# Kernel optimization log

Hardware: AMD Instinct MI355X
Metric: run time of the kernel (lower is better)

Reference implementation:

```python
import jax, jax.numpy as jnp
import numpy as np

B, T, M, P = 64, 2048, 512, 512


def setup_inputs() -> dict:
    key = jax.random.key(0)
    ks = jax.random.split(key, 9)
    s = 0.02
    return {
        "hidden_state": jax.random.normal(ks[0], (B, P), jnp.float32),
        "cell_state": jax.random.normal(ks[1], (B, P), jnp.float32),
        "encoder_h": jax.random.normal(ks[2], (B, T, M), jnp.float32),
        # Dense W_d: (2p -> m)
        "W_d": jax.random.normal(ks[3], (2 * P, M), jnp.float32) * s,
        "b_wd": jnp.zeros((M,), jnp.float32),
        # Dense U_d: (m -> m)
        "U_d": jax.random.normal(ks[4], (M, M), jnp.float32) * s,
        "b_ud": jnp.zeros((M,), jnp.float32),
        # Dense v_d: (m -> 1)
        "v_d": jax.random.normal(ks[5], (M, 1), jnp.float32) * s,
        "b_vd": jnp.zeros((1,), jnp.float32),
    }


def reference(hidden_state, cell_state, encoder_h, W_d, b_wd, U_d, b_ud, v_d, b_vd):
    # W_d(RepeatVector(T)(concat([d, s]))): the Dense is applied to the same
    # (B, 2p) vector at every time step, so compute it once and broadcast.
    ds = jnp.concatenate([hidden_state, cell_state], axis=-1)          # (B, 2p)
    ds_proj = ds @ W_d + b_wd                                          # (B, m)
    enc_proj = jnp.einsum('btm,mn->btn', encoder_h, U_d) + b_ud        # (B, T, m)
    e = jnp.tanh(ds_proj[:, None, :] + enc_proj)                       # (B, T, m)
    l = e @ v_d + b_vd                                                 # (B, T, 1)
    return jax.nn.softmax(l, axis=1)                                   # softmax over T
```

## Files before the change

### kernel.cpp

```cpp
#include <hip/hip_runtime.h>
#include <cstdint>
#include <cstddef>


typedef float  floatx4 __attribute__((ext_vector_type(4)));
typedef short  shortx8 __attribute__((ext_vector_type(8)));
typedef unsigned int uintx4 __attribute__((ext_vector_type(4)));

__device__ __forceinline__ short f2bf_rne(float f) {
  unsigned u = __float_as_uint(f);
  unsigned r = u + 0x7FFFu + ((u >> 16) & 1u);
  return (short)(r >> 16);
}

__device__ __forceinline__ unsigned pack_bf_trunc(float lo, float hi) {
  return __builtin_amdgcn_perm(__float_as_uint(hi), __float_as_uint(lo), 0x07060302u);
}

#define SB() __builtin_amdgcn_sched_barrier(0)
#define WAIT_VM0() asm volatile("s_waitcnt vmcnt(0)" ::: "memory")
#define WAIT_VM4() asm volatile("s_waitcnt vmcnt(4)" ::: "memory")
#define WAIT_VM8() asm volatile("s_waitcnt vmcnt(8)" ::: "memory")
#define WAIT_LGKM0() asm volatile("s_waitcnt lgkmcnt(0)" ::: "memory")
#define BAR() __builtin_amdgcn_s_barrier()

extern "C" __global__ __launch_bounds__(256) void prep_kernel(
    const float* __restrict__ hidden, const float* __restrict__ cell,
    const float* __restrict__ W_d, const float* __restrict__ b_wd,
    const float* __restrict__ U_d, const float* __restrict__ b_ud,
    float* __restrict__ S, short* __restrict__ UT, float* __restrict__ lzero)
{
  int bx = blockIdx.x, tid = threadIdx.x;
  if (bx < 128) {
    int idx = bx * 256 + tid;
    int b = idx >> 9, n = idx & 511;
    const float* h = hidden + b * 512;
    const float* c = cell   + b * 512;
    float a0 = b_wd[n] + b_ud[n], a1 = 0.f, a2 = 0.f, a3 = 0.f;
    for (int k = 0; k < 512; k += 4) {
      a0 = fmaf(h[k + 0], W_d[(k + 0) * 512 + n], a0);
      a1 = fmaf(h[k + 1], W_d[(k + 1) * 512 + n], a1);
      a2 = fmaf(h[k + 2], W_d[(k + 2) * 512 + n], a2);
      a3 = fmaf(h[k + 3], W_d[(k + 3) * 512 + n], a3);
    }
    for (int k = 0; k < 512; k += 4) {
      a0 = fmaf(c[k + 0], W_d[(k + 512) * 512 + n], a0);
      a1 = fmaf(c[k + 1], W_d[(k + 513) * 512 + n], a1);
      a2 = fmaf(c[k + 2], W_d[(k + 514) * 512 + n], a2);
      a3 = fmaf(c[k + 3], W_d[(k + 515) * 512 + n], a3);
    }
    S[idx] = (a0 + a1) + (a2 + a3);
  } else if (bx < 384) {
    int idx = (bx - 128) * 1024 + tid * 4;
    int n = idx >> 9, k0 = idx & 511;
    unsigned lo = (unsigned short)f2bf_rne(U_d[(size_t)(k0 + 0) * 512 + n]) |
                  ((unsigned)(unsigned short)f2bf_rne(U_d[(size_t)(k0 + 1) * 512 + n]) << 16);
    unsigned hi = (unsigned short)f2bf_rne(U_d[(size_t)(k0 + 2) * 512 + n]) |
                  ((unsigned)(unsigned short)f2bf_rne(U_d[(size_t)(k0 + 3) * 512 + n]) << 16);
    uint2 w; w.x = lo; w.y = hi;
    *(uint2*)(UT + idx) = w;
  } else {
    int idx = ((bx - 384) * 256 + tid) * 4;
    floatx4 z = {0.f, 0.f, 0.f, 0.f};
    *(floatx4*)(lzero + idx) = z;
  }
}

struct GemmState {
  short (*As)[4096];
  const float* aptr;
  const short* bfp[4];
  int afrag0, awbase;
};

template <int T>
__device__ __forceinline__ void kiter(
    GemmState& st, shortx8 (&bfr)[2][4][2], floatx4 (&areg)[4],
    floatx4 (&acc)[4][4])
{
  constexpr int CUR = T & 1;
  constexpr int NXT = CUR ^ 1;
  const short* Ab = &st.As[CUR][0];
  shortx8 af[4][2];

#pragma unroll
  for (int tr = 0; tr < 4; ++tr)
#pragma unroll
    for (int s = 0; s < 2; ++s)
      af[tr][s] = *(const shortx8*)(Ab + ((st.afrag0 + tr * 1024) ^ (s * 32)));
  SB();
  if constexpr (T < 7) {
#pragma unroll
    for (int tc = 0; tc < 4; ++tc)
#pragma unroll
      for (int s = 0; s < 2; ++s)
        bfr[NXT][tc][s] = *(const shortx8*)(st.bfp[tc] + (T + 1) * 64 + s * 32);
  }
  SB();
  WAIT_LGKM0(); SB();
  __builtin_amdgcn_s_setprio(1);
#pragma unroll
  for (int tr = 0; tr < 2; ++tr)
#pragma unroll
    for (int tc = 0; tc < 4; ++tc)
#pragma unroll
      for (int s = 0; s < 2; ++s)
        acc[tr][tc] = __builtin_amdgcn_mfma_f32_16x16x32_bf16(
            af[tr][s], bfr[CUR][tc][s], acc[tr][tc], 0, 0, 0);
  __builtin_amdgcn_s_setprio(0);
  SB();
  if constexpr (T < 7) {
    WAIT_VM8(); SB();
    short* An = &st.As[NXT][0];
    uintx4 w0, w1;
    w0.x = pack_bf_trunc(areg[0].x, areg[0].y);
    w0.y = pack_bf_trunc(areg[0].z, areg[0].w);
    w0.z = pack_bf_trunc(areg[1].x, areg[1].y);
    w0.w = pack_bf_trunc(areg[1].z, areg[1].w);
    w1.x = pack_bf_trunc(areg[2].x, areg[2].y);
    w1.y = pack_bf_trunc(areg[2].z, areg[2].w);
    w1.z = pack_bf_trunc(areg[3].x, areg[3].y);
    w1.w = pack_bf_trunc(areg[3].z, areg[3].w);
    *(uintx4*)(An + st.awbase)       = w0;
    *(uintx4*)(An + (st.awbase ^ 8)) = w1;
    SB();
  }
  if constexpr (T < 6) {
#pragma unroll
    for (int i = 0; i < 4; ++i)
      areg[i] = *(const floatx4*)(st.aptr + (T + 2) * 64 + i * 4);
  }
  SB();
  __builtin_amdgcn_s_setprio(1);
#pragma unroll
  for (int tr = 2; tr < 4; ++tr)
#pragma unroll
    for (int tc = 0; tc < 4; ++tc)
#pragma unroll
      for (int s = 0; s < 2; ++s)
        acc[tr][tc] = __builtin_amdgcn_mfma_f32_16x16x32_bf16(
            af[tr][s], bfr[CUR][tc][s], acc[tr][tc], 0, 0, 0);
  __builtin_amdgcn_s_setprio(0);
  SB();
  if constexpr (T < 7) {
    if constexpr (T < 6) { WAIT_VM4(); }
    else                 { WAIT_VM0(); }
    SB();
    WAIT_LGKM0(); SB();
    BAR(); SB();
  }
}

extern "C" __global__ __launch_bounds__(256, 2) void attn_gemm(
    const float* __restrict__ A, const short* __restrict__ UT,
    const float* __restrict__ S, const float* __restrict__ vd,
    float* __restrict__ lout)
{
  __shared__ short As[2][4096];

  const int tid = threadIdx.x;
  const int bx  = blockIdx.x;
  const int xcd = bx & 7;
  const int wg  = xcd * 512 + (bx >> 3);
  const int cb  = wg & 1;
  const int rb  = wg >> 1;
  const int row0 = rb << 6;
  const int col0 = cb << 8;
  const int lane = tid & 63;
  const int wc = tid >> 6;
  const int q = lane >> 4, l15 = lane & 15;

  GemmState st;
  st.As = As;

  const int arow = tid >> 2;
  const int akq  = tid & 3;
  st.aptr   = A + (size_t)(row0 + arow) * 512 + akq * 16;
  st.awbase = arow * 64 + (((2 * akq) ^ (arow & 7)) << 3);

#pragma unroll
  for (int tc = 0; tc < 4; ++tc)
    st.bfp[tc] = UT + (size_t)(col0 + wc * 64 + tc * 16 + l15) * 512 + q * 8;

  st.afrag0 = l15 * 64 + ((q ^ (l15 & 7)) << 3);

  floatx4 acc[4][4];
#pragma unroll
  for (int i = 0; i < 4; ++i)
#pragma unroll
    for (int j = 0; j < 4; ++j)
      acc[i][j] = (floatx4){0.f, 0.f, 0.f, 0.f};

  floatx4 areg[4];
  shortx8 bfr[2][4][2];

  SB();
#pragma unroll
  for (int i = 0; i < 4; ++i) areg[i] = *(const floatx4*)(st.aptr + i * 4);
  SB();
#pragma unroll
  for (int tc = 0; tc < 4; ++tc)
#pragma unroll
    for (int s = 0; s < 2; ++s)
      bfr[0][tc][s] = *(const shortx8*)(st.bfp[tc] + s * 32);
  SB();
  WAIT_VM8(); SB();
  {
    uintx4 w0, w1;
    w0.x = pack_bf_trunc(areg[0].x, areg[0].y);
    w0.y = pack_bf_trunc(areg[0].z, areg[0].w);
    w0.z = pack_bf_trunc(areg[1].x, areg[1].y);
    w0.w = pack_bf_trunc(areg[1].z, areg[1].w);
    w1.x = pack_bf_trunc(areg[2].x, areg[2].y);
    w1.y = pack_bf_trunc(areg[2].z, areg[2].w);
    w1.z = pack_bf_trunc(areg[3].x, areg[3].y);
    w1.w = pack_bf_trunc(areg[3].z, areg[3].w);
    *(uintx4*)(&As[0][st.awbase])       = w0;
    *(uintx4*)(&As[0][st.awbase ^ 8])   = w1;
  }
  SB();
#pragma unroll
  for (int i = 0; i < 4; ++i) areg[i] = *(const floatx4*)(st.aptr + 64 + i * 4);
  SB();
  WAIT_VM4(); SB();
  WAIT_LGKM0(); SB();
  BAR(); SB();

  kiter<0>(st, bfr, areg, acc);
  kiter<1>(st, bfr, areg, acc);
  kiter<2>(st, bfr, areg, acc);
  kiter<3>(st, bfr, areg, acc);
  kiter<4>(st, bfr, areg, acc);
  kiter<5>(st, bfr, areg, acc);
  kiter<6>(st, bfr, areg, acc);
  kiter<7>(st, bfr, areg, acc);

  const int bb = rb >> 5;
  const float* Srow = S + bb * 512;
  float sv[4], vv[4];
#pragma unroll
  for (int tc = 0; tc < 4; ++tc) {
    int n = col0 + wc * 64 + tc * 16 + l15;
    sv[tc] = Srow[n];
    vv[tc] = vd[n];
  }
#pragma unroll
  for (int tr = 0; tr < 4; ++tr) {
#pragma unroll
    for (int r = 0; r < 4; ++r) {
      float ssum = 0.f;
#pragma unroll
      for (int tc = 0; tc < 4; ++tc) {
        float x = acc[tr][tc][r] + sv[tc];
        x = fminf(15.f, fmaxf(-15.f, x));
        float e2 = __expf(2.f * x);
        float e = (e2 - 1.f) / (e2 + 1.f);
        ssum += e * vv[tc];
      }
      ssum += __shfl_xor(ssum, 1);
      ssum += __shfl_xor(ssum, 2);
      ssum += __shfl_xor(ssum, 4);
      ssum += __shfl_xor(ssum, 8);
      if (l15 == 0) {
        int row = row0 + tr * 16 + q * 4 + r;
        atomicAdd(lout + row, ssum);
      }
    }
  }
}

extern "C" __global__ __launch_bounds__(256) void softmax_t(float* __restrict__ l)
{
  int b = blockIdx.x, tid = threadIdx.x;
  int wave = tid >> 6, lane = tid & 63;
  float* row = l + (size_t)b * 2048;
  float v[8];
  float mx = -3.4e38f;
#pragma unroll
  for (int i = 0; i < 8; ++i) { v[i] = row[tid + i * 256]; mx = fmaxf(mx, v[i]); }
#pragma unroll
  for (int m = 1; m < 64; m <<= 1) mx = fmaxf(mx, __shfl_xor(mx, m));
  __shared__ float red[8];
  if (lane == 0) red[wave] = mx;
  __syncthreads();
  mx = fmaxf(fmaxf(red[0], red[1]), fmaxf(red[2], red[3]));
  float s = 0.f;
#pragma unroll
  for (int i = 0; i < 8; ++i) { v[i] = __expf(v[i] - mx); s += v[i]; }
#pragma unroll
  for (int m = 1; m < 64; m <<= 1) s += __shfl_xor(s, m);
  if (lane == 0) red[4 + wave] = s;
  __syncthreads();
  s = red[4] + red[5] + red[6] + red[7];
  float inv = 1.f / s;
#pragma unroll
  for (int i = 0; i < 8; ++i) row[tid + i * 256] = v[i] * inv;
}

extern "C" void kernel_launch(void* const* d_in, const int* in_sizes, int n_in,
                              void* d_out, int out_size, void* d_ws, size_t ws_size,
                              hipStream_t stream) {
  const float* hidden = (const float*)d_in[0];
  const float* cell   = (const float*)d_in[1];
  const float* enc    = (const float*)d_in[2];
  const float* W_d    = (const float*)d_in[3];
  const float* b_wd   = (const float*)d_in[4];
  const float* U_d    = (const float*)d_in[5];
  const float* b_ud   = (const float*)d_in[6];
  const float* v_d    = (const float*)d_in[7];
  float* out = (float*)d_out;
  float* S   = (float*)d_ws;
  short* UT  = (short*)((char*)d_ws + 32768 * sizeof(float));

  hipLaunchKernelGGL(prep_kernel, dim3(512), dim3(256), 0, stream,
                     hidden, cell, W_d, b_wd, U_d, b_ud, S, UT, out);
  hipLaunchKernelGGL(attn_gemm, dim3(4096), dim3(256), 0, stream,
                     enc, UT, S, v_d, out);
  hipLaunchKernelGGL(softmax_t, dim3(64), dim3(256), 0, stream, out);
}
```

Baseline: 502.4 us.

## Enlarge GEMM tile to 128x256 with LDS-staged B via global_load_lds

The attention GEMM block grows from 256 to 512 threads and now covers 128 rows instead of 64, so each B (U_d bf16) tile is reused across two wave-rows. B is staged through LDS with direct global-to-LDS loads, replacing the per-wave register prefetch from global memory. The prep kernel writes U_d pre-tiled and pre-swizzled so the LDS copy needs no reshuffling. A fp32 registers are now double-buffered. The goal is to cut redundant global/L2 traffic for B. The cost is 96KB of LDS per block, which likely limits occupancy, plus more complex wait-count sequencing.

Measured after the change: 528.0 us. +5.1%, slower.

```diff
diff --git a/kernel.cpp b/kernel.cpp
--- a/kernel.cpp
+++ b/kernel.cpp
@@ -16,6 +16,11 @@
 __device__ __forceinline__ unsigned pack_bf_trunc(float lo, float hi) {
   return __builtin_amdgcn_perm(__float_as_uint(hi), __float_as_uint(lo), 0x07060302u);
 }
+
+#define GLOAD_LDS16(gptr, lptr)                                                 \
+  __builtin_amdgcn_global_load_lds(                                             \
+      (const __attribute__((address_space(1))) void*)(gptr),                    \
+      (__attribute__((address_space(3))) void*)(lptr), 16, 0, 0)
 
 #define SB() __builtin_amdgcn_sched_barrier(0)
 #define WAIT_VM0() asm volatile("s_waitcnt vmcnt(0)" ::: "memory")
@@ -51,12 +56,20 @@
     }
     S[idx] = (a0 + a1) + (a2 + a3);
   } else if (bx < 384) {
-    int idx = (bx - 128) * 1024 + tid * 4;
-    int n = idx >> 9, k0 = idx & 511;
-    unsigned lo = (unsigned short)f2bf_rne(U_d[(size_t)(k0 + 0) * 512 + n]) |
-                  ((unsigned)(unsigned short)f2bf_rne(U_d[(size_t)(k0 + 1) * 512 + n]) << 16);
-    unsigned hi = (unsigned short)f2bf_rne(U_d[(size_t)(k0 + 2) * 512 + n]) |
-                  ((unsigned)(unsigned short)f2bf_rne(U_d[(size_t)(k0 + 3) * 512 + n]) << 16);
+    int idx  = (bx - 128) * 1024 + tid * 4;
+    int tile = idx >> 14;
+    int cb = tile >> 3, kt = tile & 7;
+    int sI = idx & 16383;
+    int n  = sI >> 6;
+    int gp = (sI >> 3) & 7;
+    int bb = sI & 7;
+    int gl = gp ^ (n & 7);
+    int k0 = kt * 64 + gl * 8 + bb;
+    int ng = cb * 256 + n;
+    unsigned lo = (unsigned short)f2bf_rne(U_d[(size_t)(k0 + 0) * 512 + ng]) |
+                  ((unsigned)(unsigned short)f2bf_rne(U_d[(size_t)(k0 + 1) * 512 + ng]) << 16);
+    unsigned hi = (unsigned short)f2bf_rne(U_d[(size_t)(k0 + 2) * 512 + ng]) |
+                  ((unsigned)(unsigned short)f2bf_rne(U_d[(size_t)(k0 + 3) * 512 + ng]) << 16);
     uint2 w; w.x = lo; w.y = hi;
     *(uint2*)(UT + idx) = w;
   } else {
@@ -67,35 +80,65 @@
 }
 
 struct GemmState {
-  short (*As)[4096];
+  short (*As)[8192];
+  short (*Bs)[16384];
   const float* aptr;
-  const short* bfp[4];
-  int afrag0, awbase;
+  const short* bsrc;
+  int bldsbase;
+  int afrag0, bfrag0, awbase;
 };
+
+__device__ __forceinline__ void a_pack_write(short* An, int awbase,
+                                             const floatx4* ar) {
+  uintx4 w0, w1;
+  w0.x = pack_bf_trunc(ar[0].x, ar[0].y);
+  w0.y = pack_bf_trunc(ar[0].z, ar[0].w);
+  w0.z = pack_bf_trunc(ar[1].x, ar[1].y);
+  w0.w = pack_bf_trunc(ar[1].z, ar[1].w);
+  w1.x = pack_bf_trunc(ar[2].x, ar[2].y);
+  w1.y = pack_bf_trunc(ar[2].z, ar[2].w);
+  w1.z = pack_bf_trunc(ar[3].x, ar[3].y);
+  w1.w = pack_bf_trunc(ar[3].z, ar[3].w);
+  *(uintx4*)(An + awbase)       = w0;
+  *(uintx4*)(An + (awbase ^ 8)) = w1;
+}
 
 template <int T>
 __device__ __forceinline__ void kiter(
-    GemmState& st, shortx8 (&bfr)[2][4][2], floatx4 (&areg)[4],
+    GemmState& st, floatx4 (&aregA)[4], floatx4 (&aregB)[4],
     floatx4 (&acc)[4][4])
 {
   constexpr int CUR = T & 1;
   constexpr int NXT = CUR ^ 1;
   const short* Ab = &st.As[CUR][0];
-  shortx8 af[4][2];
-
+  const short* Bb = &st.Bs[CUR][0];
+  floatx4* cons = (T & 1) ? aregA : aregB;
+  floatx4* next = (T & 1) ? aregB : aregA;
+  shortx8 af[4][2], bf[4][2];
+
+  if constexpr (T < 7) {
+#pragma unroll
+    for (int j = 0; j < 4; ++j)
+      GLOAD_LDS16(st.bsrc + (T + 1) * 16384 + j * 512,
+                  &st.Bs[NXT][st.bldsbase + j * 512]);
+  }
+  SB();
+  if constexpr (T < 6) {
+#pragma unroll
+    for (int i = 0; i < 4; ++i)
+      next[i] = *(const floatx4*)(st.aptr + (T + 2) * 64 + i * 4);
+  }
+  SB();
 #pragma unroll
   for (int tr = 0; tr < 4; ++tr)
 #pragma unroll
     for (int s = 0; s < 2; ++s)
       af[tr][s] = *(const shortx8*)(Ab + ((st.afrag0 + tr * 1024) ^ (s * 32)));
-  SB();
-  if constexpr (T < 7) {
-#pragma unroll
-    for (int tc = 0; tc < 4; ++tc)
-#pragma unroll
-      for (int s = 0; s < 2; ++s)
-        bfr[NXT][tc][s] = *(const shortx8*)(st.bfp[tc] + (T + 1) * 64 + s * 32);
-  }
+#pragma unroll
+  for (int tc = 0; tc < 4; ++tc)
+#pragma unroll
+    for (int s = 0; s < 2; ++s)
+      bf[tc][s] = *(const shortx8*)(Bb + ((st.bfrag0 + tc * 1024) ^ (s * 32)));
   SB();
   WAIT_LGKM0(); SB();
   __builtin_amdgcn_s_setprio(1);
@@ -106,31 +149,17 @@
 #pragma unroll
       for (int s = 0; s < 2; ++s)
         acc[tr][tc] = __builtin_amdgcn_mfma_f32_16x16x32_bf16(
-            af[tr][s], bfr[CUR][tc][s], acc[tr][tc], 0, 0, 0);
+            af[tr][s], bf[tc][s], acc[tr][tc], 0, 0, 0);
   __builtin_amdgcn_s_setprio(0);
   SB();
   if constexpr (T < 7) {
-    WAIT_VM8(); SB();
-    short* An = &st.As[NXT][0];
-    uintx4 w0, w1;
-    w0.x = pack_bf_trunc(areg[0].x, areg[0].y);
-    w0.y = pack_bf_trunc(areg[0].z, areg[0].w);
-    w0.z = pack_bf_trunc(areg[1].x, areg[1].y);
-    w0.w = pack_bf_trunc(areg[1].z, areg[1].w);
-    w1.x = pack_bf_trunc(areg[2].x, areg[2].y);
-    w1.y = pack_bf_trunc(areg[2].z, areg[2].w);
-    w1.z = pack_bf_trunc(areg[3].x, areg[3].y);
-    w1.w = pack_bf_trunc(areg[3].z, areg[3].w);
-    *(uintx4*)(An + st.awbase)       = w0;
-    *(uintx4*)(An + (st.awbase ^ 8)) = w1;
+    if constexpr (T < 6) { WAIT_VM8(); }
+    else                 { WAIT_VM4(); }
     SB();
-  }
-  if constexpr (T < 6) {
-#pragma unroll
-    for (int i = 0; i < 4; ++i)
-      areg[i] = *(const floatx4*)(st.aptr + (T + 2) * 64 + i * 4);
-  }
-  SB();
+    a_pack_write(&st.As[NXT][0], st.awbase, cons);
+    SB();
+  }
+  WAIT_LGKM0(); SB();
   __builtin_amdgcn_s_setprio(1);
 #pragma unroll
   for (int tr = 2; tr < 4; ++tr)
@@ -139,50 +168,53 @@
 #pragma unroll
       for (int s = 0; s < 2; ++s)
         acc[tr][tc] = __builtin_amdgcn_mfma_f32_16x16x32_bf16(
-            af[tr][s], bfr[CUR][tc][s], acc[tr][tc], 0, 0, 0);
+            af[tr][s], bf[tc][s], acc[tr][tc], 0, 0, 0);
   __builtin_amdgcn_s_setprio(0);
   SB();
   if constexpr (T < 7) {
     if constexpr (T < 6) { WAIT_VM4(); }
     else                 { WAIT_VM0(); }
     SB();
-    WAIT_LGKM0(); SB();
     BAR(); SB();
   }
 }
 
-extern "C" __global__ __launch_bounds__(256, 2) void attn_gemm(
+extern "C" __global__ __launch_bounds__(512, 2) void attn_gemm(
     const float* __restrict__ A, const short* __restrict__ UT,
     const float* __restrict__ S, const float* __restrict__ vd,
     float* __restrict__ lout)
 {
-  __shared__ short As[2][4096];
+  __shared__ short As[2][8192];
+  __shared__ short Bs[2][16384];
 
   const int tid = threadIdx.x;
   const int bx  = blockIdx.x;
   const int xcd = bx & 7;
-  const int wg  = xcd * 512 + (bx >> 3);
+  const int wg  = xcd * 256 + (bx >> 3);
   const int cb  = wg & 1;
   const int rb  = wg >> 1;
-  const int row0 = rb << 6;
+  const int row0 = rb << 7;
   const int col0 = cb << 8;
+  const int wave = tid >> 6;
   const int lane = tid & 63;
-  const int wc = tid >> 6;
+  const int wr = wave >> 2, wc = wave & 3;
   const int q = lane >> 4, l15 = lane & 15;
 
   GemmState st;
   st.As = As;
+  st.Bs = Bs;
 
   const int arow = tid >> 2;
   const int akq  = tid & 3;
   st.aptr   = A + (size_t)(row0 + arow) * 512 + akq * 16;
-  st.awbase = arow * 64 + (((2 * akq) ^ (arow & 7)) << 3);
-
-#pragma unroll
-  for (int tc = 0; tc < 4; ++tc)
-    st.bfp[tc] = UT + (size_t)(col0 + wc * 64 + tc * 16 + l15) * 512 + q * 8;
-
-  st.afrag0 = l15 * 64 + ((q ^ (l15 & 7)) << 3);
+  st.awbase = arow * 64 + (((akq * 2) ^ (arow & 7)) << 3);
+
+  st.bsrc     = UT + (size_t)cb * 131072 + wave * 2048 + lane * 8;
+  st.bldsbase = wave * 2048;
+
+  const int fgp = (q ^ (l15 & 7)) << 3;
+  st.afrag0 = (wr * 64 + l15) * 64 + fgp;
+  st.bfrag0 = (wc * 64 + l15) * 64 + fgp;
 
   floatx4 acc[4][4];
 #pragma unroll
@@ -191,51 +223,36 @@
     for (int j = 0; j < 4; ++j)
       acc[i][j] = (floatx4){0.f, 0.f, 0.f, 0.f};
 
-  floatx4 areg[4];
-  shortx8 bfr[2][4][2];
-
-  SB();
-#pragma unroll
-  for (int i = 0; i < 4; ++i) areg[i] = *(const floatx4*)(st.aptr + i * 4);
-  SB();
-#pragma unroll
-  for (int tc = 0; tc < 4; ++tc)
-#pragma unroll
-    for (int s = 0; s < 2; ++s)
-      bfr[0][tc][s] = *(const shortx8*)(st.bfp[tc] + s * 32);
-  SB();
-  WAIT_VM8(); SB();
-  {
-    uintx4 w0, w1;
-    w0.x = pack_bf_trunc(areg[0].x, areg[0].y);
-    w0.y = pack_bf_trunc(areg[0].z, areg[0].w);
-    w0.z = pack_bf_trunc(areg[1].x, areg[1].y);
-    w0.w = pack_bf_trunc(areg[1].z, areg[1].w);
-    w1.x = pack_bf_trunc(areg[2].x, areg[2].y);
-    w1.y = pack_bf_trunc(areg[2].z, areg[2].w);
-    w1.z = pack_bf_trunc(areg[3].x, areg[3].y);
-    w1.w = pack_bf_trunc(areg[3].z, areg[3].w);
-    *(uintx4*)(&As[0][st.awbase])       = w0;
-    *(uintx4*)(&As[0][st.awbase ^ 8])   = w1;
-  }
-  SB();
-#pragma unroll
-  for (int i = 0; i < 4; ++i) areg[i] = *(const floatx4*)(st.aptr + 64 + i * 4);
+  floatx4 aregA[4], aregB[4];
+
+  SB();
+#pragma unroll
+  for (int i = 0; i < 4; ++i) aregA[i] = *(const floatx4*)(st.aptr + i * 4);
+  SB();
+#pragma unroll
+  for (int j = 0; j < 4; ++j)
+    GLOAD_LDS16(st.bsrc + j * 512, &Bs[0][st.bldsbase + j * 512]);
+  SB();
+  WAIT_VM4(); SB();
+  a_pack_write(&As[0][0], st.awbase, aregA);
+  SB();
+#pragma unroll
+  for (int i = 0; i < 4; ++i) aregB[i] = *(const floatx4*)(st.aptr + 64 + i * 4);
   SB();
   WAIT_VM4(); SB();
   WAIT_LGKM0(); SB();
   BAR(); SB();
 
-  kiter<0>(st, bfr, areg, acc);
-  kiter<1>(st, bfr, areg, acc);
-  kiter<2>(st, bfr, areg, acc);
-  kiter<3>(st, bfr, areg, acc);
-  kiter<4>(st, bfr, areg, acc);
-  kiter<5>(st, bfr, areg, acc);
-  kiter<6>(st, bfr, areg, acc);
-  kiter<7>(st, bfr, areg, acc);
-
-  const int bb = rb >> 5;
+  kiter<0>(st, aregA, aregB, acc);
+  kiter<1>(st, aregA, aregB, acc);
+  kiter<2>(st, aregA, aregB, acc);
+  kiter<3>(st, aregA, aregB, acc);
+  kiter<4>(st, aregA, aregB, acc);
+  kiter<5>(st, aregA, aregB, acc);
+  kiter<6>(st, aregA, aregB, acc);
+  kiter<7>(st, aregA, aregB, acc);
+
+  const int bb = rb >> 4;
   const float* Srow = S + bb * 512;
   float sv[4], vv[4];
 #pragma unroll
@@ -262,7 +279,7 @@
       ssum += __shfl_xor(ssum, 4);
       ssum += __shfl_xor(ssum, 8);
       if (l15 == 0) {
-        int row = row0 + tr * 16 + q * 4 + r;
+        int row = row0 + wr * 64 + tr * 16 + q * 4 + r;
         atomicAdd(lout + row, ssum);
       }
     }
@@ -314,7 +331,7 @@
 
   hipLaunchKernelGGL(prep_kernel, dim3(512), dim3(256), 0, stream,
                      hidden, cell, W_d, b_wd, U_d, b_ud, S, UT, out);
-  hipLaunchKernelGGL(attn_gemm, dim3(4096), dim3(256), 0, stream,
+  hipLaunchKernelGGL(attn_gemm, dim3(2048), dim3(512), 0, stream,
                      enc, UT, S, v_d, out);
   hipLaunchKernelGGL(softmax_t, dim3(64), dim3(256), 0, stream, out);
 }
```
